# Performance work log

Hardware: AMD Instinct MI355X
Metric: run time of the kernel (lower is better)

The kernel has to match this reference:

```python
import jax, jax.numpy as jnp
import numpy as np

N, D, K_MAX = 65536, 1024, 64   # n points, feature dim, config.out_size (max #clusters)
LAMBDA = 1000.0                  # hardcoded in dpmeans.__init__
MAX_ITER = 50
OBJ_TOL = 1e-3
INF = 1e30


def setup_inputs() -> dict:
    key = jax.random.key(0)
    x = jax.random.normal(key, (1, N, D), dtype=jnp.float32)
    return {"x": x}


def _dpmeans_forward(X):
    """Faithful DP-means fit: padded to K_MAX slots, convergence via freeze flag."""
    n, d = X.shape
    mu0 = jnp.zeros((K_MAX, d), X.dtype).at[0].set(jnp.mean(X, axis=0))
    z0 = jnp.zeros((n,), jnp.int32)
    slot = jnp.arange(K_MAX)
    x2 = jnp.sum(X * X, axis=1, keepdims=True)  # (N,1), loop-invariant

    def step(carry, _):
        it, K, mu, z, prev_obj, done = carry
        # squared distance matrix via expansion (avoids N*K*D intermediate)
        m2 = jnp.sum(mu * mu, axis=1)                      # (K_MAX,)
        dist = x2 - 2.0 * (X @ mu.T) + m2[None, :]         # (N,K_MAX)
        dist = jnp.where(slot[None, :] < K, dist, INF)     # mask inactive slots
        dmin = jnp.min(dist, axis=1)
        z_new = jnp.argmin(dist, axis=1).astype(jnp.int32)
        # dynamic cluster creation: points farther than Lambda form a new cluster
        far = dmin > LAMBDA
        create = jnp.logical_and(jnp.any(far), K < K_MAX)
        Kc = jnp.minimum(K, K_MAX - 1)
        farf = far.astype(X.dtype)
        new_center = (farf @ X) / jnp.maximum(jnp.sum(farf), 1.0)   # mean of far points
        mu_new = jnp.where(create, mu.at[Kc].set(new_center), mu)
        new_col = jnp.sum((X - new_center[None, :]) ** 2, axis=1)   # dist to new center
        cf = jnp.logical_and(create, far)
        z_new = jnp.where(cf, Kc, z_new)
        dvals = jnp.where(cf, new_col, dmin)   # dist[i, z[i]] pre mean-update (as in numpy code)
        K_new = K + create.astype(K.dtype)
        # scatter-mean centroid update (empty clusters keep their center)
        counts = jax.ops.segment_sum(jnp.ones((n,), X.dtype), z_new, num_segments=K_MAX)
        sums = jax.ops.segment_sum(X, z_new, num_segments=K_MAX)
        mu_new = jnp.where((counts > 0.0)[:, None],
                           sums / jnp.maximum(counts, 1.0)[:, None], mu_new)
        obj = jnp.sum(dvals) + LAMBDA * K_new.astype(X.dtype)
        converged = jnp.logical_and(it > 0, jnp.abs(obj - prev_obj) < OBJ_TOL * obj)
        new_carry = (it + 1, K_new, mu_new, z_new, obj, jnp.logical_or(done, converged))
        # freeze state once converged (emulates early break)
        carry_out = jax.tree_util.tree_map(lambda o, nv: jnp.where(done, o, nv), carry, new_carry)
        return carry_out, None

    init = (jnp.int32(0), jnp.int32(1), mu0, z0, jnp.float32(0.0), jnp.bool_(False))
    (_, K, mu, z, _, _), _ = jax.lax.scan(step, init, None, length=MAX_ITER)
    return mu, z


def reference(x):
    X = x[0]                       # squeeze(0): (N, D)
    mu, z = _dpmeans_forward(X)
    return mu[None, :, :]          # unsqueeze(0): (1, K_MAX, D); rows >= final K are padding
```

## Files before the change

### kernel.cpp

```cpp
#include <hip/hip_runtime.h>
#include <math.h>


#define NPTS   65536
#define DDIM   1024
#define KMAX   64
#define GRID   256
#define LAMBDA_F 1000.0f
#define INF_F  1e30f

struct Scal {
  int K, it, done, _p;
  double prev_obj;
  double s_all[2], s_far[2], sx2far[2];
  int farcnt[2];
  int counts[2][64];
};


__device__ __forceinline__ void gbarO(int* cnt, int* gen) {
  __syncthreads();
  if (threadIdx.x == 0) {
    __threadfence();
    int g = __hip_atomic_load(gen, __ATOMIC_RELAXED, __HIP_MEMORY_SCOPE_AGENT);
    int a = __hip_atomic_fetch_add(cnt, 1, __ATOMIC_ACQ_REL, __HIP_MEMORY_SCOPE_AGENT);
    if (a == GRID - 1) {
      __hip_atomic_store(cnt, 0, __ATOMIC_RELAXED, __HIP_MEMORY_SCOPE_AGENT);
      __hip_atomic_store(gen, g + 1, __ATOMIC_RELEASE, __HIP_MEMORY_SCOPE_AGENT);
    } else {
      while (__hip_atomic_load(gen, __ATOMIC_ACQUIRE, __HIP_MEMORY_SCOPE_AGENT) == g)
        __builtin_amdgcn_s_sleep(2);
    }
    __threadfence();
  }
  __syncthreads();
}

__device__ __forceinline__ void gbarT(int* bar, int b, int r) {
  __syncthreads();
  if (threadIdx.x == 0) {
    __threadfence();
    int* leaf = bar + ((b >> 3) << 5);
    int v = __hip_atomic_fetch_add(leaf, 1, __ATOMIC_ACQ_REL, __HIP_MEMORY_SCOPE_AGENT);
    if (v == (r << 3) - 1) {
      int w = __hip_atomic_fetch_add(bar + 1024, 1, __ATOMIC_ACQ_REL, __HIP_MEMORY_SCOPE_AGENT);
      if (w == (r << 5) - 1)
        __hip_atomic_store(bar + 1056, r, __ATOMIC_RELEASE, __HIP_MEMORY_SCOPE_AGENT);
    }
    while (__hip_atomic_load(bar + 1056, __ATOMIC_ACQUIRE, __HIP_MEMORY_SCOPE_AGENT) < r)
      __builtin_amdgcn_s_sleep(2);
    __threadfence();
  }
  __syncthreads();
}

__global__ void kInit(int* bar) { bar[threadIdx.x] = 0; bar[1024 + threadIdx.x] = 0; }

template <int GP>
__device__ __forceinline__ void phaseAT(
    const float* __restrict__ XT, const float* __restrict__ mu,
    const float* __restrict__ x2, int* __restrict__ z,
    const float* __restrict__ m2f, Scal* sc, char* smem,
    int b, int tid, int K, int Kc, int slot) {
  constexpr int LSTR = 34;
  constexpr int LGP = (GP == 1) ? 0 : (GP == 2) ? 1 : (GP == 4) ? 2 : 3;
  constexpr int MUTOT = GP * 128;
  constexpr int MURND = (MUTOT + 255) / 256;

  float*  lX   = (float*)smem;
  float*  lMu  = (float*)(smem + 34816);
  double* wred = (double*)(smem + 43520);
  int*    wfc  = (int*)(smem + 43616);
  int*    lcnt = (int*)(smem + 43648);
  float*  rdm  = (float*)smem;
  int*    rkm  = (int*)(smem + 9216);

  const int lane = tid & 63, wv = tid >> 6;
  const int pg = tid & 31, tg = tid >> 5;
  const int kg = tg & (GP - 1);
  const int sub = tg >> LGP;
  const int pbase = b << 8;
  const int p0loc = sub * (GP << 5);
  const int jrow = tid >> 3, q = tid & 7;

  if (tid < KMAX) lcnt[tid] = 0;

  float acc[GP][8];
  #pragma unroll
  for (int i = 0; i < GP; ++i)
    #pragma unroll
    for (int j = 0; j < 8; ++j) acc[i][j] = 0.f;

  float4 xr4[8];
  float2 mr[MURND];

  #pragma unroll
  for (int i = 0; i < 8; ++i)
    xr4[i] = *(const float4*)&XT[(size_t)jrow * NPTS + pbase + (i << 5) + (q << 2)];
  #pragma unroll
  for (int r = 0; r < MURND; ++r) {
    int idx = (r << 8) + tid;
    if (idx < MUTOT) {
      int k = idx >> 4, c2 = (idx & 15) << 1;
      mr[r] = *(const float2*)&mu[(k << 10) + c2];
    }
  }

  for (int dc = 0; dc < DDIM; dc += 32) {
    __syncthreads();
    #pragma unroll
    for (int i = 0; i < 8; ++i) {
      const int p = (i << 5) + (q << 2);
      lX[(p + 0) * LSTR + jrow] = xr4[i].x;
      lX[(p + 1) * LSTR + jrow] = xr4[i].y;
      lX[(p + 2) * LSTR + jrow] = xr4[i].z;
      lX[(p + 3) * LSTR + jrow] = xr4[i].w;
    }
    #pragma unroll
    for (int r = 0; r < MURND; ++r) {
      int idx = (r << 8) + tid;
      if (idx < MUTOT) {
        int k = idx >> 4, c2 = (idx & 15) << 1;
        *(float2*)&lMu[k * LSTR + c2] = mr[r];
      }
    }
    __syncthreads();
    const int dcn = dc + 32;
    if (dcn < DDIM) {
      #pragma unroll
      for (int i = 0; i < 8; ++i)
        xr4[i] = *(const float4*)&XT[(size_t)(dcn + jrow) * NPTS + pbase + (i << 5) + (q << 2)];
      #pragma unroll
      for (int r = 0; r < MURND; ++r) {
        int idx = (r << 8) + tid;
        if (idx < MUTOT) {
          int k = idx >> 4, c2 = (idx & 15) << 1;
          mr[r] = *(const float2*)&mu[(k << 10) + dcn + c2];
        }
      }
    }
    for (int d2 = 0; d2 < 16; ++d2) {
      float2 ma[8], xa[GP];
      #pragma unroll
      for (int j = 0; j < 8; ++j)
        ma[j] = *(const float2*)&lMu[((kg << 3) + j) * LSTR + (d2 << 1)];
      #pragma unroll
      for (int i = 0; i < GP; ++i)
        xa[i] = *(const float2*)&lX[(p0loc + (i << 5) + pg) * LSTR + (d2 << 1)];
      #pragma unroll
      for (int i = 0; i < GP; ++i)
        #pragma unroll
        for (int j = 0; j < 8; ++j)
          acc[i][j] = fmaf(xa[i].y, ma[j].y, fmaf(xa[i].x, ma[j].x, acc[i][j]));
    }
  }
  __syncthreads();

  float m2v[8];
  #pragma unroll
  for (int j = 0; j < 8; ++j) m2v[j] = m2f[(kg << 3) + j];
  float x2v[GP];
  #pragma unroll
  for (int i = 0; i < GP; ++i) x2v[i] = x2[pbase + p0loc + (i << 5) + pg];

  #pragma unroll
  for (int i = 0; i < GP; ++i) {
    float bd2 = INF_F; int bk2 = KMAX;
    #pragma unroll
    for (int j = 0; j < 8; ++j) {
      int k = (kg << 3) + j;
      if (k < K) {
        float dist = x2v[i] - 2.0f * acc[i][j] + m2v[j];
        if (dist < bd2) { bd2 = dist; bk2 = k; }
      }
    }
    const int pl = p0loc + (i << 5) + pg;
    rdm[pl * 9 + kg] = bd2;
    rkm[pl * 9 + kg] = bk2;
  }
  __syncthreads();

  float bd = INF_F; int bk = KMAX;
  #pragma unroll
  for (int g = 0; g < GP; ++g) {
    float dv = rdm[tid * 9 + g]; int kv = rkm[tid * 9 + g];
    if (dv < bd || (dv == bd && kv < bk)) { bd = dv; bk = kv; }
  }

  const bool far = bd > LAMBDA_F;
  const int zf = (far && (K < KMAX)) ? Kc : bk;
  z[pbase + tid] = zf;
  atomicAdd(&lcnt[zf], 1);

  const float x2p = x2[pbase + tid];
  double a = (double)bd;
  double f = far ? (double)bd : 0.0;
  double xf = far ? (double)x2p : 0.0;
  unsigned long long bal = __ballot(far);
  int fc = __popcll(bal);
  #pragma unroll
  for (int m = 1; m < 64; m <<= 1) {
    a += __shfl_xor(a, m); f += __shfl_xor(f, m); xf += __shfl_xor(xf, m);
  }
  if (lane == 0) { wred[wv] = a; wred[4 + wv] = f; wred[8 + wv] = xf; wfc[wv] = fc; }
  __syncthreads();
  if (tid == 0) {
    unsafeAtomicAdd(&sc->s_all[slot],  wred[0] + wred[1] + wred[2] + wred[3]);
    unsafeAtomicAdd(&sc->s_far[slot],  wred[4] + wred[5] + wred[6] + wred[7]);
    unsafeAtomicAdd(&sc->sx2far[slot], wred[8] + wred[9] + wred[10] + wred[11]);
    atomicAdd(&sc->farcnt[slot], wfc[0] + wfc[1] + wfc[2] + wfc[3]);
  }
  if (tid < KMAX) {
    int c = lcnt[tid];
    if (c > 0) atomicAdd(&sc->counts[slot][tid], c);
  }
}

__global__ __launch_bounds__(256, 1) void kMainT(
    const float* __restrict__ X, float* __restrict__ mu,
    float* __restrict__ x2, int* __restrict__ z,
    double* __restrict__ sums, double* __restrict__ musum,
    float* __restrict__ m2f, Scal* sc, int* bar, float* __restrict__ XT) {
  __shared__ __align__(16) char smem[65536];
  const int tid = threadIdx.x;
  const int b = blockIdx.x;
  const int lane = tid & 63, wv = tid >> 6;
  int rnd = 0;

  sums[(b << 8) + tid] = 0.0;
  if (b == 0) {
    if (tid < 64) { sc->counts[0][tid] = 0; sc->counts[1][tid] = 0; }
    if (tid == 0) {
      sc->K = 1; sc->it = 0; sc->done = 0; sc->prev_obj = 0.0;
      for (int s2 = 0; s2 < 2; ++s2) {
        sc->s_all[s2] = 0.0; sc->s_far[s2] = 0.0; sc->sx2far[s2] = 0.0; sc->farcnt[s2] = 0;
      }
    }
  }
  if (b == 1) {
    musum[tid] = 0.0; musum[256 + tid] = 0.0;
    musum[512 + tid] = 0.0; musum[768 + tid] = 0.0;
  }
  gbarT(bar, b, ++rnd);

  {
    const int pbase = b << 8;
    for (int i = 0; i < 64; ++i) {
      const int p = pbase + (i << 2) + wv;
      const float* row = X + ((size_t)p << 10);
      float s = 0.f;
      #pragma unroll
      for (int c = 0; c < 4; ++c) {
        float4 v = *(const float4*)&row[(c << 8) + (lane << 2)];
        s += v.x * v.x + v.y * v.y + v.z * v.z + v.w * v.w;
      }
      #pragma unroll
      for (int m = 1; m < 64; m <<= 1) s += __shfl_xor(s, m);
      if (lane == 0) x2[p] = s;
    }
  }

  {
    const int pbase = b << 8;
    const int jrow = tid >> 3, q = tid & 7;
    float* lX = (float*)smem;
    for (int dc = 0; dc < DDIM; dc += 32) {
      __syncthreads();
      #pragma unroll
      for (int r = 0; r < 16; ++r) {
        int idx = (r << 8) + tid;
        int p = idx >> 4, c2 = (idx & 15) << 1;
        *(float2*)&lX[p * 34 + c2] =
            *(const float2*)&X[((size_t)(pbase + p) << 10) + dc + c2];
      }
      __syncthreads();
      #pragma unroll
      for (int i = 0; i < 8; ++i) {
        const int p = (i << 5) + (q << 2);
        float4 v;
        v.x = lX[(p + 0) * 34 + jrow];
        v.y = lX[(p + 1) * 34 + jrow];
        v.z = lX[(p + 2) * 34 + jrow];
        v.w = lX[(p + 3) * 34 + jrow];
        *(float4*)&XT[(size_t)(dc + jrow) * NPTS + pbase + p] = v;
      }
    }
  }
  gbarT(bar, b, ++rnd);

  {
    const int dcb = b & 3, nb = b >> 2;
    const int d = (dcb << 8) + tid;
    const float* xr = XT + (size_t)d * NPTS + ((size_t)nb << 10);
    float s = 0.f;
    for (int p4 = 0; p4 < 256; ++p4) {
      float4 v = *(const float4*)&xr[p4 << 2];
      s += v.x; s += v.y; s += v.z; s += v.w;
    }
    unsafeAtomicAdd(&musum[d], (double)s);
  }
  gbarT(bar, b, ++rnd);

  if (b < KMAX) {
    double* w = (double*)smem;
    const int k = b;
    if (k == 0) {
      double ss = 0.0;
      #pragma unroll
      for (int r = 0; r < 4; ++r) {
        int d = (r << 8) + tid;
        float m = (float)(musum[d] * (1.0 / 65536.0));
        mu[d] = m;
        ss += (double)m * (double)m;
      }
      #pragma unroll
      for (int mk = 1; mk < 64; mk <<= 1) ss += __shfl_xor(ss, mk);
      if (lane == 0) w[wv] = ss;
      __syncthreads();
      if (tid == 0) m2f[0] = (float)(w[0] + w[1] + w[2] + w[3]);
    } else {
      #pragma unroll
      for (int r = 0; r < 4; ++r) mu[(k << 10) + (r << 8) + tid] = 0.f;
      if (tid == 0) m2f[k] = 0.f;
    }
  }
  gbarT(bar, b, ++rnd);

  for (int t = 0; t < 50; ++t) {
    const int dn = *(volatile int*)&sc->done;
    if (dn) break;
    const int K = *(volatile int*)&sc->K;
    const int Kc = (K < KMAX - 1) ? K : (KMAX - 1);
    const int slot = t & 1;

    {
      const int gneed = (K + 7) >> 3;
      if (gneed <= 1)      phaseAT<1>(XT, mu, x2, z, m2f, sc, smem, b, tid, K, Kc, slot);
      else if (gneed <= 2) phaseAT<2>(XT, mu, x2, z, m2f, sc, smem, b, tid, K, Kc, slot);
      else if (gneed <= 4) phaseAT<4>(XT, mu, x2, z, m2f, sc, smem, b, tid, K, Kc, slot);
      else                 phaseAT<8>(XT, mu, x2, z, m2f, sc, smem, b, tid, K, Kc, slot);
    }
    gbarT(bar, b, ++rnd);

    {
      float (*accS)[256] = (float (*)[256])(void*)smem;
      const int dcb = b & 3, nb = b >> 2;
      const int p0 = nb << 10;
      #pragma unroll
      for (int k = 0; k < KMAX; ++k) accS[k][tid] = 0.f;
      __syncthreads();
      const float* xrow = XT + (size_t)((dcb << 8) + tid) * NPTS + p0;
      const int* zp = z + p0;
      #pragma unroll 8
      for (int p4 = 0; p4 < 256; ++p4) {
        float4 xc = *(const float4*)&xrow[p4 << 2];
        int4  zc = *(const int4*)&zp[p4 << 2];
        accS[zc.x][tid] += xc.x;
        accS[zc.y][tid] += xc.y;
        accS[zc.z][tid] += xc.z;
        accS[zc.w][tid] += xc.w;
      }
      __syncthreads();
      for (int k = 0; k < KMAX; ++k)
        if (sc->counts[slot][k] > 0)
          unsafeAtomicAdd(&sums[(k << 10) + (dcb << 8) + tid], (double)accS[k][tid]);
    }
    gbarT(bar, b, ++rnd);

    if (b < KMAX) {
      double* w = (double*)smem;
      const int k = b;
      const int c = sc->counts[slot][k];
      const double inv = (c > 0) ? 1.0 / (double)c : 0.0;
      double ss = 0.0;
      #pragma unroll
      for (int r = 0; r < 4; ++r) {
        int d = (r << 8) + tid;
        float m = mu[(k << 10) + d];
        if (c > 0) m = (float)(sums[(k << 10) + d] * inv);
        mu[(k << 10) + d] = m;
        sums[(k << 10) + d] = 0.0;
        ss += (double)m * (double)m;
      }
      #pragma unroll
      for (int mk = 1; mk < 64; mk <<= 1) ss += __shfl_xor(ss, mk);
      if (lane == 0) w[wv] = ss;
      __syncthreads();
      float m2k = 0.f;
      if (tid == 0) {
        m2k = (float)(w[0] + w[1] + w[2] + w[3]);
        m2f[k] = m2k;
      }
      if (k == Kc) {
        if (tid < 64) sc->counts[slot ^ 1][tid] = 0;
        if (tid == 0) {
          sc->s_all[slot ^ 1] = 0.0; sc->s_far[slot ^ 1] = 0.0;
          sc->sx2far[slot ^ 1] = 0.0; sc->farcnt[slot ^ 1] = 0;
          int farc = sc->farcnt[slot];
          int create = (farc > 0 && K < KMAX) ? 1 : 0;
          int Knew = K + create;
          double obj;
          if (create)
            obj = (sc->s_all[slot] - sc->s_far[slot]) +
                  (sc->sx2far[slot] - (double)farc * (double)m2k);
          else
            obj = sc->s_all[slot];
          obj += 1000.0 * (double)Knew;
          int conv = (sc->it > 0) && (fabs(obj - sc->prev_obj) < 1e-3 * obj);
          sc->done = conv;
          sc->prev_obj = obj;
          sc->K = Knew;
          sc->it = sc->it + 1;
        }
      }
    }
    gbarT(bar, b, ++rnd);
  }
}

template <int GP>
__device__ __forceinline__ void phaseAO(
    const float* __restrict__ X, const float* __restrict__ mu,
    const float* __restrict__ x2, int* __restrict__ z,
    const float* __restrict__ m2f, Scal* sc, char* smem,
    int b, int tid, int K, int Kc, int slot) {
  constexpr int LSTR = 34;
  constexpr int LGP = (GP == 1) ? 0 : (GP == 2) ? 1 : (GP == 4) ? 2 : 3;
  constexpr int MUTOT = GP * 128;
  constexpr int MURND = (MUTOT + 255) / 256;

  float*  lX   = (float*)smem;
  float*  lMu  = (float*)(smem + 34816);
  double* wred = (double*)(smem + 43520);
  int*    wfc  = (int*)(smem + 43616);
  int*    lcnt = (int*)(smem + 43648);
  float*  rdm  = (float*)smem;
  int*    rkm  = (int*)(smem + 9216);

  const int lane = tid & 63, wv = tid >> 6;
  const int pg = tid & 31, tg = tid >> 5;
  const int kg = tg & (GP - 1);
  const int sub = tg >> LGP;
  const int pbase = b << 8;
  const int p0loc = sub * (GP << 5);

  if (tid < KMAX) lcnt[tid] = 0;

  float acc[GP][8];
  #pragma unroll
  for (int i = 0; i < GP; ++i)
    #pragma unroll
    for (int j = 0; j < 8; ++j) acc[i][j] = 0.f;

  float2 xr[16];
  float2 mr[MURND];

  #pragma unroll
  for (int r = 0; r < 16; ++r) {
    int idx = (r << 8) + tid;
    int p = idx >> 4, c2 = (idx & 15) << 1;
    xr[r] = *(const float2*)&X[((size_t)(pbase + p) << 10) + c2];
  }
  #pragma unroll
  for (int r = 0; r < MURND; ++r) {
    int idx = (r << 8) + tid;
    if (idx < MUTOT) {
      int k = idx >> 4, c2 = (idx & 15) << 1;
      mr[r] = *(const float2*)&mu[(k << 10) + c2];
    }
  }

  for (int dc = 0; dc < DDIM; dc += 32) {
    __syncthreads();
    #pragma unroll
    for (int r = 0; r < 16; ++r) {
      int idx = (r << 8) + tid;
      int p = idx >> 4, c2 = (idx & 15) << 1;
      *(float2*)&lX[p * LSTR + c2] = xr[r];
    }
    #pragma unroll
    for (int r = 0; r < MURND; ++r) {
      int idx = (r << 8) + tid;
      if (idx < MUTOT) {
        int k = idx >> 4, c2 = (idx & 15) << 1;
        *(float2*)&lMu[k * LSTR + c2] = mr[r];
      }
    }
    __syncthreads();
    const int dcn = dc + 32;
    if (dcn < DDIM) {
      #pragma unroll
      for (int r = 0; r < 16; ++r) {
        int idx = (r << 8) + tid;
        int p = idx >> 4, c2 = (idx & 15) << 1;
        xr[r] = *(const float2*)&X[((size_t)(pbase + p) << 10) + dcn + c2];
      }
      #pragma unroll
      for (int r = 0; r < MURND; ++r) {
        int idx = (r << 8) + tid;
// ... 182 lines not shown
      __syncthreads();
      const float* xp = X + ((size_t)p0 << 10) + (dcb << 8) + tid;
      const int* zp = z + p0;
      for (int p = 0; p < 1024; ++p)
        accS[zp[p]][tid] += xp[(size_t)p << 10];
      __syncthreads();
      for (int k = 0; k < KMAX; ++k)
        if (sc->counts[slot][k] > 0)
          unsafeAtomicAdd(&sums[(k << 10) + (dcb << 8) + tid], (double)accS[k][tid]);
    }
    gbarO(bcnt, bgen);

    if (b < KMAX) {
      double* w = (double*)smem;
      const int k = b;
      const int c = sc->counts[slot][k];
      const double inv = (c > 0) ? 1.0 / (double)c : 0.0;
      double ss = 0.0;
      #pragma unroll
      for (int r = 0; r < 4; ++r) {
        int d = (r << 8) + tid;
        float m = mu[(k << 10) + d];
        if (c > 0) m = (float)(sums[(k << 10) + d] * inv);
        mu[(k << 10) + d] = m;
        sums[(k << 10) + d] = 0.0;
        ss += (double)m * (double)m;
      }
      #pragma unroll
      for (int mk = 1; mk < 64; mk <<= 1) ss += __shfl_xor(ss, mk);
      if (lane == 0) w[wv] = ss;
      __syncthreads();
      float m2k = 0.f;
      if (tid == 0) {
        m2k = (float)(w[0] + w[1] + w[2] + w[3]);
        m2f[k] = m2k;
      }
      if (k == Kc) {
        if (tid < 64) sc->counts[slot ^ 1][tid] = 0;
        if (tid == 0) {
          sc->s_all[slot ^ 1] = 0.0; sc->s_far[slot ^ 1] = 0.0;
          sc->sx2far[slot ^ 1] = 0.0; sc->farcnt[slot ^ 1] = 0;
          int farc = sc->farcnt[slot];
          int create = (farc > 0 && K < KMAX) ? 1 : 0;
          int Knew = K + create;
          double obj;
          if (create)
            obj = (sc->s_all[slot] - sc->s_far[slot]) +
                  (sc->sx2far[slot] - (double)farc * (double)m2k);
          else
            obj = sc->s_all[slot];
          obj += 1000.0 * (double)Knew;
          int conv = (sc->it > 0) && (fabs(obj - sc->prev_obj) < 1e-3 * obj);
          sc->done = conv;
          sc->prev_obj = obj;
          sc->K = Knew;
          sc->it = sc->it + 1;
        }
      }
    }
    gbarO(bcnt, bgen);
  }
}


extern "C" void kernel_launch(void* const* d_in, const int* in_sizes, int n_in,
                              void* d_out, int out_size, void* d_ws, size_t ws_size,
                              hipStream_t stream) {
  const float* X = (const float*)d_in[0];
  float* mu = (float*)d_out;
  char* ws = (char*)d_ws;
  float*  x2    = (float*)(ws + 0);
  int*    z     = (int*)(ws + 262144);
  double* sums  = (double*)(ws + 524288);
  double* musum = (double*)(ws + 1048576);
  float*  m2f   = (float*)(ws + 1056768);
  Scal*   sc    = (Scal*)(ws + 1057024);
  int*    bar   = (int*)(ws + 1058048);
  float*  XT    = (float*)(ws + (size_t)(2u << 20));

  const size_t need = (size_t)(2u << 20) + (size_t)DDIM * NPTS * sizeof(float);

  kInit<<<1, 1024, 0, stream>>>(bar);
  if (ws_size >= need)
    kMainT<<<GRID, 256, 0, stream>>>(X, mu, x2, z, sums, musum, m2f, sc, bar, XT);
  else
    kMainOld<<<GRID, 256, 0, stream>>>(X, mu, x2, z, sums, musum, m2f, sc, bar);
}
```

Before: 1.128 ms.

## Double threads per block to 512 and split distance GEMM tile across them

```diff
diff --git a/kernel.cpp b/kernel.cpp
--- a/kernel.cpp
+++ b/kernel.cpp
@@ -57,21 +57,22 @@
 __global__ void kInit(int* bar) { bar[threadIdx.x] = 0; bar[1024 + threadIdx.x] = 0; }
 
 template <int GP>
-__device__ __forceinline__ void phaseAT(
+__device__ __forceinline__ void phaseA512(
     const float* __restrict__ XT, const float* __restrict__ mu,
     const float* __restrict__ x2, int* __restrict__ z,
     const float* __restrict__ m2f, Scal* sc, char* smem,
     int b, int tid, int K, int Kc, int slot) {
   constexpr int LSTR = 34;
-  constexpr int LGP = (GP == 1) ? 0 : (GP == 2) ? 1 : (GP == 4) ? 2 : 3;
+  constexpr int LGP = (GP == 2) ? 1 : (GP == 4) ? 2 : 3;
+  constexpr int GPH = GP / 2;
   constexpr int MUTOT = GP * 128;
-  constexpr int MURND = (MUTOT + 255) / 256;
+  constexpr int MURND = (MUTOT + 511) / 512;
 
   float*  lX   = (float*)smem;
   float*  lMu  = (float*)(smem + 34816);
   double* wred = (double*)(smem + 43520);
-  int*    wfc  = (int*)(smem + 43616);
-  int*    lcnt = (int*)(smem + 43648);
+  int*    wfc  = (int*)(smem + 43712);
+  int*    lcnt = (int*)(smem + 43744);
   float*  rdm  = (float*)smem;
   int*    rkm  = (int*)(smem + 9216);
 
@@ -80,26 +81,28 @@
   const int kg = tg & (GP - 1);
   const int sub = tg >> LGP;
   const int pbase = b << 8;
-  const int p0loc = sub * (GP << 5);
-  const int jrow = tid >> 3, q = tid & 7;
+  const int p0loc = sub * (GP << 4);
+  const int jrow = tid >> 4, q16 = tid & 15;
+  const int kact_lim = ((K + 7) >> 3) << 3;
+  const bool kact = (kg << 3) < kact_lim;
 
   if (tid < KMAX) lcnt[tid] = 0;
 
-  float acc[GP][8];
-  #pragma unroll
-  for (int i = 0; i < GP; ++i)
+  float acc[GPH][8];
+  #pragma unroll
+  for (int i = 0; i < GPH; ++i)
     #pragma unroll
     for (int j = 0; j < 8; ++j) acc[i][j] = 0.f;
 
-  float4 xr4[8];
+  float4 xr4[4];
   float2 mr[MURND];
 
   #pragma unroll
-  for (int i = 0; i < 8; ++i)
-    xr4[i] = *(const float4*)&XT[(size_t)jrow * NPTS + pbase + (i << 5) + (q << 2)];
+  for (int i = 0; i < 4; ++i)
+    xr4[i] = *(const float4*)&XT[(size_t)jrow * NPTS + pbase + (i << 6) + (q16 << 2)];
   #pragma unroll
   for (int r = 0; r < MURND; ++r) {
-    int idx = (r << 8) + tid;
+    int idx = (r << 9) + tid;
     if (idx < MUTOT) {
       int k = idx >> 4, c2 = (idx & 15) << 1;
       mr[r] = *(const float2*)&mu[(k << 10) + c2];
@@ -109,8 +112,8 @@
   for (int dc = 0; dc < DDIM; dc += 32) {
     __syncthreads();
     #pragma unroll
-    for (int i = 0; i < 8; ++i) {
-      const int p = (i << 5) + (q << 2);
+    for (int i = 0; i < 4; ++i) {
+      const int p = (i << 6) + (q16 << 2);
       lX[(p + 0) * LSTR + jrow] = xr4[i].x;
       lX[(p + 1) * LSTR + jrow] = xr4[i].y;
       lX[(p + 2) * LSTR + jrow] = xr4[i].z;
@@ -118,7 +121,7 @@
     }
     #pragma unroll
     for (int r = 0; r < MURND; ++r) {
-      int idx = (r << 8) + tid;
+      int idx = (r << 9) + tid;
       if (idx < MUTOT) {
         int k = idx >> 4, c2 = (idx & 15) << 1;
         *(float2*)&lMu[k * LSTR + c2] = mr[r];
@@ -128,30 +131,32 @@
     const int dcn = dc + 32;
     if (dcn < DDIM) {
       #pragma unroll
-      for (int i = 0; i < 8; ++i)
-        xr4[i] = *(const float4*)&XT[(size_t)(dcn + jrow) * NPTS + pbase + (i << 5) + (q << 2)];
+      for (int i = 0; i < 4; ++i)
+        xr4[i] = *(const float4*)&XT[(size_t)(dcn + jrow) * NPTS + pbase + (i << 6) + (q16 << 2)];
       #pragma unroll
       for (int r = 0; r < MURND; ++r) {
-        int idx = (r << 8) + tid;
+        int idx = (r << 9) + tid;
         if (idx < MUTOT) {
           int k = idx >> 4, c2 = (idx & 15) << 1;
           mr[r] = *(const float2*)&mu[(k << 10) + dcn + c2];
         }
       }
     }
-    for (int d2 = 0; d2 < 16; ++d2) {
-      float2 ma[8], xa[GP];
-      #pragma unroll
-      for (int j = 0; j < 8; ++j)
-        ma[j] = *(const float2*)&lMu[((kg << 3) + j) * LSTR + (d2 << 1)];
-      #pragma unroll
-      for (int i = 0; i < GP; ++i)
-        xa[i] = *(const float2*)&lX[(p0loc + (i << 5) + pg) * LSTR + (d2 << 1)];
-      #pragma unroll
-      for (int i = 0; i < GP; ++i)
+    if (kact) {
+      for (int d2 = 0; d2 < 16; ++d2) {
+        float2 ma[8], xa[GPH];
         #pragma unroll
         for (int j = 0; j < 8; ++j)
-          acc[i][j] = fmaf(xa[i].y, ma[j].y, fmaf(xa[i].x, ma[j].x, acc[i][j]));
+          ma[j] = *(const float2*)&lMu[((kg << 3) + j) * LSTR + (d2 << 1)];
+        #pragma unroll
+        for (int i = 0; i < GPH; ++i)
+          xa[i] = *(const float2*)&lX[(p0loc + (i << 5) + pg) * LSTR + (d2 << 1)];
+        #pragma unroll
+        for (int i = 0; i < GPH; ++i)
+          #pragma unroll
+          for (int j = 0; j < 8; ++j)
+            acc[i][j] = fmaf(xa[i].y, ma[j].y, fmaf(xa[i].x, ma[j].x, acc[i][j]));
+      }
     }
   }
   __syncthreads();
@@ -159,12 +164,12 @@
   float m2v[8];
   #pragma unroll
   for (int j = 0; j < 8; ++j) m2v[j] = m2f[(kg << 3) + j];
-  float x2v[GP];
-  #pragma unroll
-  for (int i = 0; i < GP; ++i) x2v[i] = x2[pbase + p0loc + (i << 5) + pg];
-
-  #pragma unroll
-  for (int i = 0; i < GP; ++i) {
+  float x2v[GPH];
+  #pragma unroll
+  for (int i = 0; i < GPH; ++i) x2v[i] = x2[pbase + p0loc + (i << 5) + pg];
+
+  #pragma unroll
+  for (int i = 0; i < GPH; ++i) {
     float bd2 = INF_F; int bk2 = KMAX;
     #pragma unroll
     for (int j = 0; j < 8; ++j) {
@@ -180,34 +185,35 @@
   }
   __syncthreads();
 
-  float bd = INF_F; int bk = KMAX;
-  #pragma unroll
-  for (int g = 0; g < GP; ++g) {
-    float dv = rdm[tid * 9 + g]; int kv = rkm[tid * 9 + g];
-    if (dv < bd || (dv == bd && kv < bk)) { bd = dv; bk = kv; }
-  }
-
-  const bool far = bd > LAMBDA_F;
-  const int zf = (far && (K < KMAX)) ? Kc : bk;
-  z[pbase + tid] = zf;
-  atomicAdd(&lcnt[zf], 1);
-
-  const float x2p = x2[pbase + tid];
-  double a = (double)bd;
-  double f = far ? (double)bd : 0.0;
-  double xf = far ? (double)x2p : 0.0;
+  float bd = INF_F; int bk = KMAX; bool far = false;
+  double a = 0.0, f = 0.0, xf = 0.0;
+  if (tid < 256) {
+    #pragma unroll
+    for (int g = 0; g < GP; ++g) {
+      float dv = rdm[tid * 9 + g]; int kv = rkm[tid * 9 + g];
+      if (dv < bd || (dv == bd && kv < bk)) { bd = dv; bk = kv; }
+    }
+    far = bd > LAMBDA_F;
+    const int zf = (far && (K < KMAX)) ? Kc : bk;
+    z[pbase + tid] = zf;
+    atomicAdd(&lcnt[zf], 1);
+    const float x2p = x2[pbase + tid];
+    a = (double)bd;
+    f = far ? (double)bd : 0.0;
+    xf = far ? (double)x2p : 0.0;
+  }
   unsigned long long bal = __ballot(far);
   int fc = __popcll(bal);
   #pragma unroll
   for (int m = 1; m < 64; m <<= 1) {
     a += __shfl_xor(a, m); f += __shfl_xor(f, m); xf += __shfl_xor(xf, m);
   }
-  if (lane == 0) { wred[wv] = a; wred[4 + wv] = f; wred[8 + wv] = xf; wfc[wv] = fc; }
+  if (lane == 0) { wred[wv] = a; wred[8 + wv] = f; wred[16 + wv] = xf; wfc[wv] = fc; }
   __syncthreads();
   if (tid == 0) {
     unsafeAtomicAdd(&sc->s_all[slot],  wred[0] + wred[1] + wred[2] + wred[3]);
-    unsafeAtomicAdd(&sc->s_far[slot],  wred[4] + wred[5] + wred[6] + wred[7]);
-    unsafeAtomicAdd(&sc->sx2far[slot], wred[8] + wred[9] + wred[10] + wred[11]);
+    unsafeAtomicAdd(&sc->s_far[slot],  wred[8] + wred[9] + wred[10] + wred[11]);
+    unsafeAtomicAdd(&sc->sx2far[slot], wred[16] + wred[17] + wred[18] + wred[19]);
     atomicAdd(&sc->farcnt[slot], wfc[0] + wfc[1] + wfc[2] + wfc[3]);
   }
   if (tid < KMAX) {
@@ -216,7 +222,7 @@
   }
 }
 
-__global__ __launch_bounds__(256, 1) void kMainT(
+__global__ __launch_bounds__(512, 2) void kMain512(
     const float* __restrict__ X, float* __restrict__ mu,
     float* __restrict__ x2, int* __restrict__ z,
     double* __restrict__ sums, double* __restrict__ musum,
@@ -227,7 +233,10 @@
   const int lane = tid & 63, wv = tid >> 6;
   int rnd = 0;
 
-  sums[(b << 8) + tid] = 0.0;
+  {
+    int si = (b << 9) + tid;
+    if (si < 65536) sums[si] = 0.0;
+  }
   if (b == 0) {
     if (tid < 64) { sc->counts[0][tid] = 0; sc->counts[1][tid] = 0; }
     if (tid == 0) {
@@ -237,16 +246,13 @@
       }
     }
   }
-  if (b == 1) {
-    musum[tid] = 0.0; musum[256 + tid] = 0.0;
-    musum[512 + tid] = 0.0; musum[768 + tid] = 0.0;
-  }
+  if (b == 1) { musum[tid] = 0.0; musum[512 + tid] = 0.0; }
   gbarT(bar, b, ++rnd);
 
   {
     const int pbase = b << 8;
-    for (int i = 0; i < 64; ++i) {
-      const int p = pbase + (i << 2) + wv;
+    for (int i = 0; i < 32; ++i) {
+      const int p = pbase + (i << 3) + wv;
       const float* row = X + ((size_t)p << 10);
       float s = 0.f;
       #pragma unroll
@@ -262,21 +268,21 @@
 
   {
     const int pbase = b << 8;
-    const int jrow = tid >> 3, q = tid & 7;
+    const int jrow = tid >> 4, q16 = tid & 15;
     float* lX = (float*)smem;
     for (int dc = 0; dc < DDIM; dc += 32) {
       __syncthreads();
       #pragma unroll
-      for (int r = 0; r < 16; ++r) {
-        int idx = (r << 8) + tid;
+      for (int r = 0; r < 8; ++r) {
+        int idx = (r << 9) + tid;
         int p = idx >> 4, c2 = (idx & 15) << 1;
         *(float2*)&lX[p * 34 + c2] =
             *(const float2*)&X[((size_t)(pbase + p) << 10) + dc + c2];
       }
       __syncthreads();
       #pragma unroll
-      for (int i = 0; i < 8; ++i) {
-        const int p = (i << 5) + (q << 2);
+      for (int i = 0; i < 4; ++i) {
+        const int p = (i << 6) + (q16 << 2);
         float4 v;
         v.x = lX[(p + 0) * 34 + jrow];
         v.y = lX[(p + 1) * 34 + jrow];
@@ -288,7 +294,7 @@
   }
   gbarT(bar, b, ++rnd);
 
-  {
+  if (tid < 256) {
     const int dcb = b & 3, nb = b >> 2;
     const int d = (dcb << 8) + tid;
     const float* xr = XT + (size_t)d * NPTS + ((size_t)nb << 10);
@@ -306,12 +312,14 @@
     const int k = b;
     if (k == 0) {
       double ss = 0.0;
-      #pragma unroll
-      for (int r = 0; r < 4; ++r) {
-        int d = (r << 8) + tid;
-        float m = (float)(musum[d] * (1.0 / 65536.0));
-        mu[d] = m;
-        ss += (double)m * (double)m;
+      if (tid < 256) {
+        #pragma unroll
+        for (int r = 0; r < 4; ++r) {
+          int d = (r << 8) + tid;
+          float m = (float)(musum[d] * (1.0 / 65536.0));
+          mu[d] = m;
+          ss += (double)m * (double)m;
+        }
       }
       #pragma unroll
       for (int mk = 1; mk < 64; mk <<= 1) ss += __shfl_xor(ss, mk);
@@ -319,8 +327,10 @@
       __syncthreads();
       if (tid == 0) m2f[0] = (float)(w[0] + w[1] + w[2] + w[3]);
     } else {
-      #pragma unroll
-      for (int r = 0; r < 4; ++r) mu[(k << 10) + (r << 8) + tid] = 0.f;
+      if (tid < 256) {
+        #pragma unroll
+        for (int r = 0; r < 4; ++r) mu[(k << 10) + (r << 8) + tid] = 0.f;
+      }
       if (tid == 0) m2f[k] = 0.f;
     }
   }
@@ -335,10 +345,9 @@
 
     {
       const int gneed = (K + 7) >> 3;
-      if (gneed <= 1)      phaseAT<1>(XT, mu, x2, z, m2f, sc, smem, b, tid, K, Kc, slot);
-      else if (gneed <= 2) phaseAT<2>(XT, mu, x2, z, m2f, sc, smem, b, tid, K, Kc, slot);
-      else if (gneed <= 4) phaseAT<4>(XT, mu, x2, z, m2f, sc, smem, b, tid, K, Kc, slot);
-      else                 phaseAT<8>(XT, mu, x2, z, m2f, sc, smem, b, tid, K, Kc, slot);
+      if (gneed <= 2)      phaseA512<2>(XT, mu, x2, z, m2f, sc, smem, b, tid, K, Kc, slot);
+      else if (gneed <= 4) phaseA512<4>(XT, mu, x2, z, m2f, sc, smem, b, tid, K, Kc, slot);
+      else                 phaseA512<8>(XT, mu, x2, z, m2f, sc, smem, b, tid, K, Kc, slot);
     }
     gbarT(bar, b, ++rnd);
 
@@ -346,24 +355,30 @@
       float (*accS)[256] = (float (*)[256])(void*)smem;
       const int dcb = b & 3, nb = b >> 2;
       const int p0 = nb << 10;
-      #pragma unroll
-      for (int k = 0; k < KMAX; ++k) accS[k][tid] = 0.f;
-      __syncthreads();
-      const float* xrow = XT + (size_t)((dcb << 8) + tid) * NPTS + p0;
-      const int* zp = z + p0;
-      #pragma unroll 8
-      for (int p4 = 0; p4 < 256; ++p4) {
-        float4 xc = *(const float4*)&xrow[p4 << 2];
-        int4  zc = *(const int4*)&zp[p4 << 2];
-        accS[zc.x][tid] += xc.x;
-        accS[zc.y][tid] += xc.y;
-        accS[zc.z][tid] += xc.z;
-        accS[zc.w][tid] += xc.w;
-      }
-      __syncthreads();
-      for (int k = 0; k < KMAX; ++k)
-        if (sc->counts[slot][k] > 0)
-          unsafeAtomicAdd(&sums[(k << 10) + (dcb << 8) + tid], (double)accS[k][tid]);
+      if (tid < 256) {
+        #pragma unroll
+        for (int k = 0; k < KMAX; ++k) accS[k][tid] = 0.f;
+      }
+      __syncthreads();
+      if (tid < 256) {
+        const float* xrow = XT + (size_t)((dcb << 8) + tid) * NPTS + p0;
+        const int* zp = z + p0;
+        #pragma unroll 8
+        for (int p4 = 0; p4 < 256; ++p4) {
+          float4 xc = *(const float4*)&xrow[p4 << 2];
+          int4  zc = *(const int4*)&zp[p4 << 2];
+          accS[zc.x][tid] += xc.x;
+          accS[zc.y][tid] += xc.y;
+          accS[zc.z][tid] += xc.z;
+          accS[zc.w][tid] += xc.w;
+        }
+      }
+      __syncthreads();
+      if (tid < 256) {
+        for (int k = 0; k < KMAX; ++k)
+          if (sc->counts[slot][k] > 0)
+            unsafeAtomicAdd(&sums[(k << 10) + (dcb << 8) + tid], (double)accS[k][tid]);
+      }
     }
     gbarT(bar, b, ++rnd);
 
@@ -373,14 +388,16 @@
       const int c = sc->counts[slot][k];
       const double inv = (c > 0) ? 1.0 / (double)c : 0.0;
       double ss = 0.0;
-      #pragma unroll
-      for (int r = 0; r < 4; ++r) {
-        int d = (r << 8) + tid;
-        float m = mu[(k << 10) + d];
-        if (c > 0) m = (float)(sums[(k << 10) + d] * inv);
-        mu[(k << 10) + d] = m;
-        sums[(k << 10) + d] = 0.0;
-        ss += (double)m * (double)m;
+      if (tid < 256) {
+        #pragma unroll
+        for (int r = 0; r < 4; ++r) {
+          int d = (r << 8) + tid;
+          float m = mu[(k << 10) + d];
+          if (c > 0) m = (float)(sums[(k << 10) + d] * inv);
+          mu[(k << 10) + d] = m;
+          sums[(k << 10) + d] = 0.0;
+          ss += (double)m * (double)m;
+        }
       }
       #pragma unroll
       for (int mk = 1; mk < 64; mk <<= 1) ss += __shfl_xor(ss, mk);
@@ -763,7 +780,7 @@
 
   kInit<<<1, 1024, 0, stream>>>(bar);
   if (ws_size >= need)
-    kMainT<<<GRID, 256, 0, stream>>>(X, mu, x2, z, sums, musum, m2f, sc, bar, XT);
+    kMain512<<<GRID, 512, 0, stream>>>(X, mu, x2, z, sums, musum, m2f, sc, bar, XT);
   else
     kMainOld<<<GRID, 256, 0, stream>>>(X, mu, x2, z, sums, musum, m2f, sc, bar);
 }
```

Result: slower. 1.252 ms (+11.0%).

## Double persistent grid to 512 blocks with 128 points per block

Applied to the files above, without the earlier changes.

```diff
diff --git a/kernel.cpp b/kernel.cpp
--- a/kernel.cpp
+++ b/kernel.cpp
@@ -5,6 +5,7 @@
 #define NPTS   65536
 #define DDIM   1024
 #define KMAX   64
+#define GRIDP  512
 #define GRID   256
 #define LAMBDA_F 1000.0f
 #define INF_F  1e30f
@@ -36,13 +37,13 @@
   __syncthreads();
 }
 
-__device__ __forceinline__ void gbarT(int* bar, int b, int r) {
+__device__ __forceinline__ void gbarP(int* bar, int b, int r) {
   __syncthreads();
   if (threadIdx.x == 0) {
     __threadfence();
-    int* leaf = bar + ((b >> 3) << 5);
+    int* leaf = bar + ((b >> 4) << 5);
     int v = __hip_atomic_fetch_add(leaf, 1, __ATOMIC_ACQ_REL, __HIP_MEMORY_SCOPE_AGENT);
-    if (v == (r << 3) - 1) {
+    if (v == (r << 4) - 1) {
       int w = __hip_atomic_fetch_add(bar + 1024, 1, __ATOMIC_ACQ_REL, __HIP_MEMORY_SCOPE_AGENT);
       if (w == (r << 5) - 1)
         __hip_atomic_store(bar + 1056, r, __ATOMIC_RELEASE, __HIP_MEMORY_SCOPE_AGENT);
@@ -56,47 +57,49 @@
 
 __global__ void kInit(int* bar) { bar[threadIdx.x] = 0; bar[1024 + threadIdx.x] = 0; }
 
-template <int GP>
-__device__ __forceinline__ void phaseAT(
+template <int NKG>
+__device__ __forceinline__ void phaseAP(
     const float* __restrict__ XT, const float* __restrict__ mu,
     const float* __restrict__ x2, int* __restrict__ z,
     const float* __restrict__ m2f, Scal* sc, char* smem,
     int b, int tid, int K, int Kc, int slot) {
   constexpr int LSTR = 34;
-  constexpr int LGP = (GP == 1) ? 0 : (GP == 2) ? 1 : (GP == 4) ? 2 : 3;
-  constexpr int MUTOT = GP * 128;
+  constexpr int NK2 = 2 * NKG;
+  constexpr int MUTOT = NK2 * 16;
   constexpr int MURND = (MUTOT + 255) / 256;
 
   float*  lX   = (float*)smem;
-  float*  lMu  = (float*)(smem + 34816);
-  double* wred = (double*)(smem + 43520);
-  int*    wfc  = (int*)(smem + 43616);
-  int*    lcnt = (int*)(smem + 43648);
+  float*  lMu  = (float*)(smem + 17408);
+  double* wred = (double*)(smem + 26112);
+  int*    wfc  = (int*)(smem + 26208);
+  int*    lcnt = (int*)(smem + 26240);
   float*  rdm  = (float*)smem;
-  int*    rkm  = (int*)(smem + 9216);
+  int*    rkm  = (int*)(smem + 1024);
 
   const int lane = tid & 63, wv = tid >> 6;
   const int pg = tid & 31, tg = tid >> 5;
-  const int kg = tg & (GP - 1);
-  const int sub = tg >> LGP;
-  const int pbase = b << 8;
-  const int p0loc = sub * (GP << 5);
+  const int kg = tg & 1, sub = tg >> 1;
+  const int pbase = b << 7;
+  const int pt = (sub << 5) + pg;
   const int jrow = tid >> 3, q = tid & 7;
+  const bool kact = (kg * NKG) < K;
 
   if (tid < KMAX) lcnt[tid] = 0;
 
-  float acc[GP][8];
-  #pragma unroll
-  for (int i = 0; i < GP; ++i)
-    #pragma unroll
-    for (int j = 0; j < 8; ++j) acc[i][j] = 0.f;
-
-  float4 xr4[8];
+  float acc[NKG];
+  #pragma unroll
+  for (int j = 0; j < NKG; ++j) acc[j] = 0.f;
+
+  float4 xr4[2];
   float2 mr[MURND];
 
   #pragma unroll
-  for (int i = 0; i < 8; ++i)
-    xr4[i] = *(const float4*)&XT[(size_t)jrow * NPTS + pbase + (i << 5) + (q << 2)];
+  for (int i = 0; i < 2; ++i)
+    xr4[i] = *(const float4*)&XT[(size_t)jrow * NPTS + pbase + (i << 6) + (q << 3) + 0];
+  float4 xr4b[2];
+  #pragma unroll
+  for (int i = 0; i < 2; ++i)
+    xr4b[i] = *(const float4*)&XT[(size_t)jrow * NPTS + pbase + (i << 6) + (q << 3) + 4];
   #pragma unroll
   for (int r = 0; r < MURND; ++r) {
     int idx = (r << 8) + tid;
@@ -109,12 +112,16 @@
   for (int dc = 0; dc < DDIM; dc += 32) {
     __syncthreads();
     #pragma unroll
-    for (int i = 0; i < 8; ++i) {
-      const int p = (i << 5) + (q << 2);
+    for (int i = 0; i < 2; ++i) {
+      const int p = (i << 6) + (q << 3);
       lX[(p + 0) * LSTR + jrow] = xr4[i].x;
       lX[(p + 1) * LSTR + jrow] = xr4[i].y;
       lX[(p + 2) * LSTR + jrow] = xr4[i].z;
       lX[(p + 3) * LSTR + jrow] = xr4[i].w;
+      lX[(p + 4) * LSTR + jrow] = xr4b[i].x;
+      lX[(p + 5) * LSTR + jrow] = xr4b[i].y;
+      lX[(p + 6) * LSTR + jrow] = xr4b[i].z;
+      lX[(p + 7) * LSTR + jrow] = xr4b[i].w;
     }
     #pragma unroll
     for (int r = 0; r < MURND; ++r) {
@@ -128,8 +135,11 @@
     const int dcn = dc + 32;
     if (dcn < DDIM) {
       #pragma unroll
-      for (int i = 0; i < 8; ++i)
-        xr4[i] = *(const float4*)&XT[(size_t)(dcn + jrow) * NPTS + pbase + (i << 5) + (q << 2)];
+      for (int i = 0; i < 2; ++i)
+        xr4[i] = *(const float4*)&XT[(size_t)(dcn + jrow) * NPTS + pbase + (i << 6) + (q << 3) + 0];
+      #pragma unroll
+      for (int i = 0; i < 2; ++i)
+        xr4b[i] = *(const float4*)&XT[(size_t)(dcn + jrow) * NPTS + pbase + (i << 6) + (q << 3) + 4];
       #pragma unroll
       for (int r = 0; r < MURND; ++r) {
         int idx = (r << 8) + tid;
@@ -139,63 +149,54 @@
         }
       }
     }
-    for (int d2 = 0; d2 < 16; ++d2) {
-      float2 ma[8], xa[GP];
-      #pragma unroll
-      for (int j = 0; j < 8; ++j)
-        ma[j] = *(const float2*)&lMu[((kg << 3) + j) * LSTR + (d2 << 1)];
-      #pragma unroll
-      for (int i = 0; i < GP; ++i)
-        xa[i] = *(const float2*)&lX[(p0loc + (i << 5) + pg) * LSTR + (d2 << 1)];
-      #pragma unroll
-      for (int i = 0; i < GP; ++i)
+    if (kact) {
+      for (int d2 = 0; d2 < 16; ++d2) {
+        float2 xa = *(const float2*)&lX[pt * LSTR + (d2 << 1)];
         #pragma unroll
-        for (int j = 0; j < 8; ++j)
-          acc[i][j] = fmaf(xa[i].y, ma[j].y, fmaf(xa[i].x, ma[j].x, acc[i][j]));
-    }
-  }
-  __syncthreads();
-
-  float m2v[8];
-  #pragma unroll
-  for (int j = 0; j < 8; ++j) m2v[j] = m2f[(kg << 3) + j];
-  float x2v[GP];
-  #pragma unroll
-  for (int i = 0; i < GP; ++i) x2v[i] = x2[pbase + p0loc + (i << 5) + pg];
-
-  #pragma unroll
-  for (int i = 0; i < GP; ++i) {
+        for (int j = 0; j < NKG; ++j) {
+          float2 mv = *(const float2*)&lMu[(kg * NKG + j) * LSTR + (d2 << 1)];
+          acc[j] = fmaf(xa.y, mv.y, fmaf(xa.x, mv.x, acc[j]));
+        }
+      }
+    }
+  }
+  __syncthreads();
+
+  {
+    const float x2v = x2[pbase + pt];
     float bd2 = INF_F; int bk2 = KMAX;
+    if (kact) {
+      #pragma unroll
+      for (int j = 0; j < NKG; ++j) {
+        int k = kg * NKG + j;
+        if (k < K) {
+          float dist = x2v - 2.0f * acc[j] + m2f[k];
+          if (dist < bd2) { bd2 = dist; bk2 = k; }
+        }
+      }
+    }
+    rdm[(pt << 1) + kg] = bd2;
+    rkm[(pt << 1) + kg] = bk2;
+  }
+  __syncthreads();
+
+  float bd = INF_F; int bk = KMAX; bool far = false;
+  double a = 0.0, f = 0.0, xf = 0.0;
+  if (tid < 128) {
     #pragma unroll
-    for (int j = 0; j < 8; ++j) {
-      int k = (kg << 3) + j;
-      if (k < K) {
-        float dist = x2v[i] - 2.0f * acc[i][j] + m2v[j];
-        if (dist < bd2) { bd2 = dist; bk2 = k; }
-      }
-    }
-    const int pl = p0loc + (i << 5) + pg;
-    rdm[pl * 9 + kg] = bd2;
-    rkm[pl * 9 + kg] = bk2;
-  }
-  __syncthreads();
-
-  float bd = INF_F; int bk = KMAX;
-  #pragma unroll
-  for (int g = 0; g < GP; ++g) {
-    float dv = rdm[tid * 9 + g]; int kv = rkm[tid * 9 + g];
-    if (dv < bd || (dv == bd && kv < bk)) { bd = dv; bk = kv; }
-  }
-
-  const bool far = bd > LAMBDA_F;
-  const int zf = (far && (K < KMAX)) ? Kc : bk;
-  z[pbase + tid] = zf;
-  atomicAdd(&lcnt[zf], 1);
-
-  const float x2p = x2[pbase + tid];
-  double a = (double)bd;
-  double f = far ? (double)bd : 0.0;
-  double xf = far ? (double)x2p : 0.0;
+    for (int g = 0; g < 2; ++g) {
+      float dv = rdm[(tid << 1) + g]; int kv = rkm[(tid << 1) + g];
+      if (dv < bd || (dv == bd && kv < bk)) { bd = dv; bk = kv; }
+    }
+    far = bd > LAMBDA_F;
+    const int zf = (far && (K < KMAX)) ? Kc : bk;
+    z[pbase + tid] = zf;
+    atomicAdd(&lcnt[zf], 1);
+    const float x2p = x2[pbase + tid];
+    a = (double)bd;
+    f = far ? (double)bd : 0.0;
+    xf = far ? (double)x2p : 0.0;
+  }
   unsigned long long bal = __ballot(far);
   int fc = __popcll(bal);
   #pragma unroll
@@ -216,18 +217,18 @@
   }
 }
 
-__global__ __launch_bounds__(256, 1) void kMainT(
+__global__ __launch_bounds__(256, 2) void kMainP(
     const float* __restrict__ X, float* __restrict__ mu,
     float* __restrict__ x2, int* __restrict__ z,
     double* __restrict__ sums, double* __restrict__ musum,
     float* __restrict__ m2f, Scal* sc, int* bar, float* __restrict__ XT) {
-  __shared__ __align__(16) char smem[65536];
+  __shared__ __align__(16) char smem[33024];
   const int tid = threadIdx.x;
   const int b = blockIdx.x;
   const int lane = tid & 63, wv = tid >> 6;
   int rnd = 0;
 
-  sums[(b << 8) + tid] = 0.0;
+  if (b < 256) sums[(b << 8) + tid] = 0.0;
   if (b == 0) {
     if (tid < 64) { sc->counts[0][tid] = 0; sc->counts[1][tid] = 0; }
     if (tid == 0) {
@@ -241,11 +242,11 @@
     musum[tid] = 0.0; musum[256 + tid] = 0.0;
     musum[512 + tid] = 0.0; musum[768 + tid] = 0.0;
   }
-  gbarT(bar, b, ++rnd);
+  gbarP(bar, b, ++rnd);
 
   {
-    const int pbase = b << 8;
-    for (int i = 0; i < 64; ++i) {
+    const int pbase = b << 7;
+    for (int i = 0; i < 32; ++i) {
       const int p = pbase + (i << 2) + wv;
       const float* row = X + ((size_t)p << 10);
       float s = 0.f;
@@ -261,13 +262,13 @@
   }
 
   {
-    const int pbase = b << 8;
+    const int pbase = b << 7;
     const int jrow = tid >> 3, q = tid & 7;
     float* lX = (float*)smem;
     for (int dc = 0; dc < DDIM; dc += 32) {
       __syncthreads();
       #pragma unroll
-      for (int r = 0; r < 16; ++r) {
+      for (int r = 0; r < 8; ++r) {
         int idx = (r << 8) + tid;
         int p = idx >> 4, c2 = (idx & 15) << 1;
         *(float2*)&lX[p * 34 + c2] =
@@ -275,20 +276,25 @@
       }
       __syncthreads();
       #pragma unroll
-      for (int i = 0; i < 8; ++i) {
-        const int p = (i << 5) + (q << 2);
-        float4 v;
-        v.x = lX[(p + 0) * 34 + jrow];
-        v.y = lX[(p + 1) * 34 + jrow];
-        v.z = lX[(p + 2) * 34 + jrow];
-        v.w = lX[(p + 3) * 34 + jrow];
+      for (int i = 0; i < 2; ++i) {
+        const int p = (i << 6) + (q << 3);
+        float4 v, v2;
+        v.x  = lX[(p + 0) * 34 + jrow];
+        v.y  = lX[(p + 1) * 34 + jrow];
+        v.z  = lX[(p + 2) * 34 + jrow];
+        v.w  = lX[(p + 3) * 34 + jrow];
+        v2.x = lX[(p + 4) * 34 + jrow];
+        v2.y = lX[(p + 5) * 34 + jrow];
+        v2.z = lX[(p + 6) * 34 + jrow];
+        v2.w = lX[(p + 7) * 34 + jrow];
         *(float4*)&XT[(size_t)(dc + jrow) * NPTS + pbase + p] = v;
-      }
-    }
-  }
-  gbarT(bar, b, ++rnd);
-
-  {
+        *(float4*)&XT[(size_t)(dc + jrow) * NPTS + pbase + p + 4] = v2;
+      }
+    }
+  }
+  gbarP(bar, b, ++rnd);
+
+  if (b < 256) {
     const int dcb = b & 3, nb = b >> 2;
     const int d = (dcb << 8) + tid;
     const float* xr = XT + (size_t)d * NPTS + ((size_t)nb << 10);
@@ -299,7 +305,7 @@
     }
     unsafeAtomicAdd(&musum[d], (double)s);
   }
-  gbarT(bar, b, ++rnd);
+  gbarP(bar, b, ++rnd);
 
   if (b < KMAX) {
     double* w = (double*)smem;
@@ -324,7 +330,7 @@
       if (tid == 0) m2f[k] = 0.f;
     }
   }
-  gbarT(bar, b, ++rnd);
+  gbarP(bar, b, ++rnd);
 
   for (int t = 0; t < 50; ++t) {
     const int dn = *(volatile int*)&sc->done;
@@ -333,39 +339,42 @@
     const int Kc = (K < KMAX - 1) ? K : (KMAX - 1);
     const int slot = t & 1;
 
+    if (K <= 8)       phaseAP<4>(XT, mu, x2, z, m2f, sc, smem, b, tid, K, Kc, slot);
+    else if (K <= 16) phaseAP<8>(XT, mu, x2, z, m2f, sc, smem, b, tid, K, Kc, slot);
+    else if (K <= 32) phaseAP<16>(XT, mu, x2, z, m2f, sc, smem, b, tid, K, Kc, slot);
+    else              phaseAP<32>(XT, mu, x2, z, m2f, sc, smem, b, tid, K, Kc, slot);
+    gbarP(bar, b, ++rnd);
+
     {
-      const int gneed = (K + 7) >> 3;
-      if (gneed <= 1)      phaseAT<1>(XT, mu, x2, z, m2f, sc, smem, b, tid, K, Kc, slot);
-      else if (gneed <= 2) phaseAT<2>(XT, mu, x2, z, m2f, sc, smem, b, tid, K, Kc, slot);
-      else if (gneed <= 4) phaseAT<4>(XT, mu, x2, z, m2f, sc, smem, b, tid, K, Kc, slot);
-      else                 phaseAT<8>(XT, mu, x2, z, m2f, sc, smem, b, tid, K, Kc, slot);
-    }
-    gbarT(bar, b, ++rnd);
-
-    {
-      float (*accS)[256] = (float (*)[256])(void*)smem;
-      const int dcb = b & 3, nb = b >> 2;
+      float (*accS)[128] = (float (*)[128])(void*)smem;
+      const int dcb = b & 7, nb = b >> 3;
       const int p0 = nb << 10;
-      #pragma unroll
-      for (int k = 0; k < KMAX; ++k) accS[k][tid] = 0.f;
-      __syncthreads();
-      const float* xrow = XT + (size_t)((dcb << 8) + tid) * NPTS + p0;
-      const int* zp = z + p0;
-      #pragma unroll 8
-      for (int p4 = 0; p4 < 256; ++p4) {
-        float4 xc = *(const float4*)&xrow[p4 << 2];
-        int4  zc = *(const int4*)&zp[p4 << 2];
-        accS[zc.x][tid] += xc.x;
-        accS[zc.y][tid] += xc.y;
-        accS[zc.z][tid] += xc.z;
-        accS[zc.w][tid] += xc.w;
-      }
-      __syncthreads();
-      for (int k = 0; k < KMAX; ++k)
-        if (sc->counts[slot][k] > 0)
-          unsafeAtomicAdd(&sums[(k << 10) + (dcb << 8) + tid], (double)accS[k][tid]);
-    }
-    gbarT(bar, b, ++rnd);
+      if (tid < 128) {
+        #pragma unroll
+        for (int k = 0; k < KMAX; ++k) accS[k][tid] = 0.f;
+      }
+      __syncthreads();
+      if (tid < 128) {
+        const float* xrow = XT + (size_t)((dcb << 7) + tid) * NPTS + p0;
+        const int* zp = z + p0;
+        #pragma unroll 8
+        for (int p4 = 0; p4 < 256; ++p4) {
+          float4 xc = *(const float4*)&xrow[p4 << 2];
+          int4  zc = *(const int4*)&zp[p4 << 2];
+          accS[zc.x][tid] += xc.x;
+          accS[zc.y][tid] += xc.y;
+          accS[zc.z][tid] += xc.z;
+          accS[zc.w][tid] += xc.w;
+        }
+      }
+      __syncthreads();
+      if (tid < 128) {
+        for (int k = 0; k < KMAX; ++k)
+          if (sc->counts[slot][k] > 0)
+            unsafeAtomicAdd(&sums[(k << 10) + (dcb << 7) + tid], (double)accS[k][tid]);
+      }
+    }
+    gbarP(bar, b, ++rnd);
 
     if (b < KMAX) {
       double* w = (double*)smem;
@@ -414,7 +423,7 @@
         }
       }
     }
-    gbarT(bar, b, ++rnd);
+    gbarP(bar, b, ++rnd);
   }
 }
 
@@ -763,7 +772,7 @@
 
   kInit<<<1, 1024, 0, stream>>>(bar);
   if (ws_size >= need)
-    kMainT<<<GRID, 256, 0, stream>>>(X, mu, x2, z, sums, musum, m2f, sc, bar, XT);
+    kMainP<<<GRIDP, 256, 0, stream>>>(X, mu, x2, z, sums, musum, m2f, sc, bar, XT);
   else
     kMainOld<<<GRID, 256, 0, stream>>>(X, mu, x2, z, sums, musum, m2f, sc, bar);
 }
```

Result: slower. 1.468 ms (+30.1%).

## Fuse x2 and mean into transpose pass, run-length accumulate sums, drop barrier fences

Applied to the files above, without the earlier changes.

```diff
diff --git a/kernel.cpp b/kernel.cpp
--- a/kernel.cpp
+++ b/kernel.cpp
@@ -39,7 +39,6 @@
 __device__ __forceinline__ void gbarT(int* bar, int b, int r) {
   __syncthreads();
   if (threadIdx.x == 0) {
-    __threadfence();
     int* leaf = bar + ((b >> 3) << 5);
     int v = __hip_atomic_fetch_add(leaf, 1, __ATOMIC_ACQ_REL, __HIP_MEMORY_SCOPE_AGENT);
     if (v == (r << 3) - 1) {
@@ -49,7 +48,6 @@
     }
     while (__hip_atomic_load(bar + 1056, __ATOMIC_ACQUIRE, __HIP_MEMORY_SCOPE_AGENT) < r)
       __builtin_amdgcn_s_sleep(2);
-    __threadfence();
   }
   __syncthreads();
 }
@@ -245,25 +243,9 @@
 
   {
     const int pbase = b << 8;
-    for (int i = 0; i < 64; ++i) {
-      const int p = pbase + (i << 2) + wv;
-      const float* row = X + ((size_t)p << 10);
-      float s = 0.f;
-      #pragma unroll
-      for (int c = 0; c < 4; ++c) {
-        float4 v = *(const float4*)&row[(c << 8) + (lane << 2)];
-        s += v.x * v.x + v.y * v.y + v.z * v.z + v.w * v.w;
-      }
-      #pragma unroll
-      for (int m = 1; m < 64; m <<= 1) s += __shfl_xor(s, m);
-      if (lane == 0) x2[p] = s;
-    }
-  }
-
-  {
-    const int pbase = b << 8;
     const int jrow = tid >> 3, q = tid & 7;
     float* lX = (float*)smem;
+    float x2acc = 0.f;
     for (int dc = 0; dc < DDIM; dc += 32) {
       __syncthreads();
       #pragma unroll
@@ -274,6 +256,7 @@
             *(const float2*)&X[((size_t)(pbase + p) << 10) + dc + c2];
       }
       __syncthreads();
+      float ms = 0.f;
       #pragma unroll
       for (int i = 0; i < 8; ++i) {
         const int p = (i << 5) + (q << 2);
@@ -283,21 +266,18 @@
         v.z = lX[(p + 2) * 34 + jrow];
         v.w = lX[(p + 3) * 34 + jrow];
         *(float4*)&XT[(size_t)(dc + jrow) * NPTS + pbase + p] = v;
-      }
-    }
-  }
-  gbarT(bar, b, ++rnd);
-
-  {
-    const int dcb = b & 3, nb = b >> 2;
-    const int d = (dcb << 8) + tid;
-    const float* xr = XT + (size_t)d * NPTS + ((size_t)nb << 10);
-    float s = 0.f;
-    for (int p4 = 0; p4 < 256; ++p4) {
-      float4 v = *(const float4*)&xr[p4 << 2];
-      s += v.x; s += v.y; s += v.z; s += v.w;
-    }
-    unsafeAtomicAdd(&musum[d], (double)s);
+        ms += v.x; ms += v.y; ms += v.z; ms += v.w;
+      }
+      #pragma unroll
+      for (int m = 1; m < 8; m <<= 1) ms += __shfl_xor(ms, m);
+      if (q == 0) unsafeAtomicAdd(&musum[dc + jrow], (double)ms);
+      #pragma unroll
+      for (int c = 0; c < 32; ++c) {
+        float v = lX[tid * 34 + c];
+        x2acc = fmaf(v, v, x2acc);
+      }
+    }
+    x2[pbase + tid] = x2acc;
   }
   gbarT(bar, b, ++rnd);
 
@@ -351,15 +331,18 @@
       __syncthreads();
       const float* xrow = XT + (size_t)((dcb << 8) + tid) * NPTS + p0;
       const int* zp = z + p0;
-      #pragma unroll 8
+      int kcur = zp[0];
+      float acc = 0.f;
+      #pragma unroll 4
       for (int p4 = 0; p4 < 256; ++p4) {
         float4 xc = *(const float4*)&xrow[p4 << 2];
         int4  zc = *(const int4*)&zp[p4 << 2];
-        accS[zc.x][tid] += xc.x;
-        accS[zc.y][tid] += xc.y;
-        accS[zc.z][tid] += xc.z;
-        accS[zc.w][tid] += xc.w;
-      }
+        if (zc.x != kcur) { accS[kcur][tid] += acc; kcur = zc.x; acc = xc.x; } else acc += xc.x;
+        if (zc.y != kcur) { accS[kcur][tid] += acc; kcur = zc.y; acc = xc.y; } else acc += xc.y;
+        if (zc.z != kcur) { accS[kcur][tid] += acc; kcur = zc.z; acc = xc.z; } else acc += xc.z;
+        if (zc.w != kcur) { accS[kcur][tid] += acc; kcur = zc.w; acc = xc.w; } else acc += xc.w;
+      }
+      accS[kcur][tid] += acc;
       __syncthreads();
       for (int k = 0; k < KMAX; ++k)
         if (sc->counts[slot][k] > 0)
```

Result: faster. 1.063 ms (-5.8%).
